# Kernel optimization log

Hardware: AMD Instinct MI355X
Metric: run time of the kernel (lower is better)

Reference implementation:

```python
import jax, jax.numpy as jnp
import numpy as np
from jax import lax

VOCAB = 12000
EMB = 512
RNN = 512
FEATS = 4096
SEQ_LEN = 15


def setup_inputs() -> dict:
    key = jax.random.key(0)
    ks = jax.random.split(key, 10)
    B = 1024
    s = 0.05
    return {
        "img_features": jax.random.normal(ks[0], (B, FEATS), jnp.float32),
        "W_feats": jax.random.normal(ks[1], (EMB, FEATS), jnp.float32) * s,
        "b_feats": jax.random.normal(ks[2], (EMB,), jnp.float32) * s,
        "W_ih": jax.random.normal(ks[3], (4 * RNN, EMB), jnp.float32) * s,
        "W_hh": jax.random.normal(ks[4], (4 * RNN, RNN), jnp.float32) * s,
        "b_ih": jax.random.normal(ks[5], (4 * RNN,), jnp.float32) * s,
        "b_hh": jax.random.normal(ks[6], (4 * RNN,), jnp.float32) * s,
        "emb": jax.random.normal(ks[7], (VOCAB, EMB), jnp.float32) * s,
        "W_out": jax.random.normal(ks[8], (VOCAB - 2, RNN), jnp.float32) * s,
        "b_out": jax.random.normal(ks[9], (VOCAB - 2,), jnp.float32) * s,
    }


def reference(img_features, W_feats, b_feats, W_ih, W_hh, b_ih, b_hh, emb, W_out, b_out):
    B = img_features.shape[0]

    def lstm_cell(x, h, c):
        # torch.nn.LSTMCell: gates ordered i, f, g, o
        gates = x @ W_ih.T + b_ih + h @ W_hh.T + b_hh
        i, f, g, o = jnp.split(gates, 4, axis=1)
        c_new = jax.nn.sigmoid(f) * c + jax.nn.sigmoid(i) * jnp.tanh(g)
        h_new = jax.nn.sigmoid(o) * jnp.tanh(c_new)
        return h_new, c_new

    # image feature embedding + ReLU, then prime the LSTM with it
    img_vec = jax.nn.relu(img_features @ W_feats.T + b_feats)  # [B, 512]
    h = jnp.zeros((B, RNN), img_features.dtype)
    c = jnp.zeros((B, RNN), img_features.dtype)
    h, c = lstm_cell(img_vec, h, c)

    def step(carry, _):
        h, c, words = carry
        x = emb[words]                     # [B, 512] embedding lookup
        h, c = lstm_cell(x, h, c)
        logits = h @ W_out.T + b_out       # [B, VOCAB-2]
        idx = jnp.argmax(logits, axis=1).astype(jnp.int32)
        return (h, c, idx + 2), idx

    words0 = jnp.ones((B,), jnp.int32)  # START token = 1
    _, seq = lax.scan(step, (h, c, words0), None, length=SEQ_LEN)
    return seq.T  # [B, SEQ_LEN] greedy-decoded token ids
```

## Files before the change

### kernel.cpp

```cpp
#include <hip/hip_runtime.h>
#include <stdint.h>

#define BATCH  1024
#define SEQLEN 15
#define NGATE  2048
#define NVOCAB 11998
#define FEATS  4096

typedef __attribute__((ext_vector_type(8)))  short  s8v;
typedef __attribute__((ext_vector_type(16))) float  f32x16;
typedef __attribute__((ext_vector_type(8)))  unsigned short us8;

__device__ __forceinline__ unsigned short f2bf(float f) {
    unsigned u = __float_as_uint(f);
    u += 0x7FFFu + ((u >> 16) & 1u);
    return (unsigned short)(u >> 16);
}
__device__ __forceinline__ float bf2f(unsigned short h) {
    return __uint_as_float(((unsigned)h) << 16);
}
struct bfpair { unsigned short hi, lo; };
__device__ __forceinline__ bfpair split2v(float v) {
    bfpair r;
    r.hi = f2bf(v);
    r.lo = f2bf(v - bf2f(r.hi));
    return r;
}
__device__ __forceinline__ void split8(const float* __restrict__ s, us8& vh, us8& vl) {
    #pragma unroll
    for (int e = 0; e < 8; ++e) {
        bfpair q = split2v(s[e]);
        vh[e] = q.hi; vl[e] = q.lo;
    }
}

__device__ __forceinline__ void async_cp16(const void* g, void* l) {
    __builtin_amdgcn_global_load_lds(
        (const __attribute__((address_space(1))) unsigned int*)g,
        (__attribute__((address_space(3))) unsigned int*)l, 16, 0, 0);
}

__global__ void prep_wcat_blk(const float* __restrict__ W_ih, const float* __restrict__ W_hh,
                              const float* __restrict__ b_ih, const float* __restrict__ b_hh,
                              unsigned short* __restrict__ hi, unsigned short* __restrict__ lo,
                              float* __restrict__ bsum) {
    int idx = blockIdx.x * 256 + threadIdx.x;
    int kc = idx >> 11, row = idx & 2047;
    int k = kc << 3;
    const float* src = (k < 512) ? (W_ih + (size_t)row * 512 + k)
                                 : (W_hh + (size_t)row * 512 + (k - 512));
    us8 vh, vl; split8(src, vh, vl);
    *(us8*)(hi + (size_t)idx * 8) = vh;
    *(us8*)(lo + (size_t)idx * 8) = vl;
    if (idx < NGATE) bsum[idx] = b_ih[idx] + b_hh[idx];
}

__global__ void prep_blk(const float* __restrict__ src,
                         unsigned short* __restrict__ hi, unsigned short* __restrict__ lo,
                         int R, int K) {
    int row = blockIdx.x * 256 + threadIdx.x;
    if (row >= R) return;
    int kc = blockIdx.y;
    us8 vh, vl; split8(src + (size_t)row * K + (kc << 3), vh, vl);
    size_t o = ((size_t)kc * R + row) * 8;
    *(us8*)(hi + o) = vh;
    *(us8*)(lo + o) = vl;
}

__device__ __forceinline__ void mfma_blk_store(
    const unsigned short* __restrict__ Ahi, const unsigned short* __restrict__ Alo, int aRows,
    const unsigned short* __restrict__ Bhi, const unsigned short* __restrict__ Blo, int bRows,
    float* __restrict__ C, int ldc,
    int K, size_t akstride, size_t bkstride, size_t czstride,
    int bm, int bn, int kz)
{
    __shared__ short smem[4 * 4 * 128 * 8];
    short* sAhi = smem;
    short* sAlo = smem + 4 * 128 * 8;
    short* sBhi = smem + 2 * 4 * 128 * 8;
    short* sBlo = smem + 3 * 4 * 128 * 8;

    Ahi += (size_t)kz * akstride;  Alo += (size_t)kz * akstride;
    Bhi += (size_t)kz * bkstride;  Blo += (size_t)kz * bkstride;
    C   += (size_t)kz * czstride;

    const int tid  = threadIdx.x;
    const int lane = tid & 63, wave = tid >> 6;
    const int wr = (wave & 1) * 64, wc = (wave >> 1) * 64;
    const int col = lane & 31, kh = lane >> 5;

    f32x16 acc[2][2] = {};

    for (int k0 = 0; k0 < K; k0 += 32) {
        const int kc0 = k0 >> 3;
        __syncthreads();
        #pragma unroll
        for (int p = 0; p < 2; ++p) {
            int s    = p * 4 + wave;
            int kc_l = s >> 1, rh = s & 1;
            int rl   = rh * 64 + lane;
            int lo_  = (kc_l * 128 + rh * 64) * 8;
            size_t ga = ((size_t)(kc0 + kc_l) * aRows + (bm + rl)) * 8;
            async_cp16(Ahi + ga, sAhi + lo_);
            async_cp16(Alo + ga, sAlo + lo_);
            int brow = bn + rl; if (brow > bRows - 1) brow = bRows - 1;
            size_t gb = ((size_t)(kc0 + kc_l) * bRows + brow) * 8;
            async_cp16(Bhi + gb, sBhi + lo_);
            async_cp16(Blo + gb, sBlo + lo_);
        }
        __syncthreads();

        #pragma unroll
        for (int st = 0; st < 2; ++st) {
            int off = (2 * st + kh) * 128 * 8;
            s8v ah0 = *(const s8v*)(sAhi + off + (wr + col) * 8);
            s8v ah1 = *(const s8v*)(sAhi + off + (wr + 32 + col) * 8);
            s8v al0 = *(const s8v*)(sAlo + off + (wr + col) * 8);
            s8v al1 = *(const s8v*)(sAlo + off + (wr + 32 + col) * 8);
            s8v bh0 = *(const s8v*)(sBhi + off + (wc + col) * 8);
            s8v bh1 = *(const s8v*)(sBhi + off + (wc + 32 + col) * 8);
            s8v bl0 = *(const s8v*)(sBlo + off + (wc + col) * 8);
            s8v bl1 = *(const s8v*)(sBlo + off + (wc + 32 + col) * 8);
            acc[0][0] = __builtin_amdgcn_mfma_f32_32x32x16_bf16(ah0, bh0, acc[0][0], 0, 0, 0);
            acc[0][1] = __builtin_amdgcn_mfma_f32_32x32x16_bf16(ah0, bh1, acc[0][1], 0, 0, 0);
            acc[1][0] = __builtin_amdgcn_mfma_f32_32x32x16_bf16(ah1, bh0, acc[1][0], 0, 0, 0);
            acc[1][1] = __builtin_amdgcn_mfma_f32_32x32x16_bf16(ah1, bh1, acc[1][1], 0, 0, 0);
            acc[0][0] = __builtin_amdgcn_mfma_f32_32x32x16_bf16(ah0, bl0, acc[0][0], 0, 0, 0);
            acc[0][1] = __builtin_amdgcn_mfma_f32_32x32x16_bf16(ah0, bl1, acc[0][1], 0, 0, 0);
            acc[1][0] = __builtin_amdgcn_mfma_f32_32x32x16_bf16(ah1, bl0, acc[1][0], 0, 0, 0);
            acc[1][1] = __builtin_amdgcn_mfma_f32_32x32x16_bf16(ah1, bl1, acc[1][1], 0, 0, 0);
            acc[0][0] = __builtin_amdgcn_mfma_f32_32x32x16_bf16(al0, bh0, acc[0][0], 0, 0, 0);
            acc[0][1] = __builtin_amdgcn_mfma_f32_32x32x16_bf16(al0, bh1, acc[0][1], 0, 0, 0);
            acc[1][0] = __builtin_amdgcn_mfma_f32_32x32x16_bf16(al1, bh0, acc[1][0], 0, 0, 0);
            acc[1][1] = __builtin_amdgcn_mfma_f32_32x32x16_bf16(al1, bh1, acc[1][1], 0, 0, 0);
        }
    }

    #pragma unroll
    for (int i = 0; i < 2; ++i)
        #pragma unroll
        for (int rg = 0; rg < 4; ++rg)
            #pragma unroll
            for (int rr = 0; rr < 4; ++rr) {
                int reg = rg * 4 + rr;
                int m = bm + wr + i * 32 + rr + rg * 8 + kh * 4;
                #pragma unroll
                for (int j = 0; j < 2; ++j) {
                    int n = bn + wc + j * 32 + col;
                    if (n < bRows) C[(size_t)m * ldc + n] = acc[i][j][reg];
                }
            }
}

template<int PPX>
__global__ __launch_bounds__(256) void k_gemm_gates(
    const unsigned short* Ahi, const unsigned short* Alo,
    const unsigned short* Bhi, const unsigned short* Blo,
    float* C, size_t aks, size_t bks, size_t czs) {
    const int l = blockIdx.x, r = l & 7, q = l >> 3;
    const int p = r * PPX + (q >> 3);
    const int mblk = q & 7, nblk = p & 15, kz = p >> 4;
    mfma_blk_store(Ahi, Alo, 1024, Bhi, Blo, NGATE, C, NGATE, 512, aks, bks, czs,
                   mblk * 128, nblk * 128, kz);
}
__global__ __launch_bounds__(256) void k_gemm_feats(
    const unsigned short* Ahi, const unsigned short* Alo,
    const unsigned short* Bhi, const unsigned short* Blo,
    float* C) {
    const int l = blockIdx.x, r = l & 7, q = l >> 3;
    const int p = r * 4 + (q >> 3);
    const int mblk = q & 7, nblk = p & 3, kz = p >> 2;
    mfma_blk_store(Ahi, Alo, 1024, Bhi, Blo, 512, C, 512, 512,
                   (size_t)64 * 1024 * 8, (size_t)64 * 512 * 8, (size_t)1024 * 512,
                   mblk * 128, nblk * 128, kz);
}

__global__ __launch_bounds__(256, 3) void k_logits_argmax(
    const unsigned short* __restrict__ h_hi, const unsigned short* __restrict__ h_lo,
    const unsigned short* __restrict__ wout_hi, const unsigned short* __restrict__ wout_lo,
    const float* __restrict__ bias, unsigned long long* __restrict__ packed)
{
    __shared__ short sB[2][2][4][128][8];

    int mblk, nblk;
    {
        const int l = blockIdx.x, r = l & 7, q = l >> 3;
        if (q < 88) { nblk = r * 11 + (q >> 3); mblk = q & 7; }
        else        { nblk = 88 + (q - 88);     mblk = r;     }
    }

    const int tid  = threadIdx.x;
    const int lane = tid & 63, wave = tid >> 6;
    const int wm = wave & 1, wn = wave >> 1;
    const int col = lane & 31, kh = lane >> 5;
    const int bm = mblk * 128, bn = nblk * 128;
    const int aRows = 1024, bRows = NVOCAB;

    f32x16 acc[2][2] = {};

    auto stage_B = [&](int kcbase, int bufi) {
        #pragma unroll
        for (int p = 0; p < 4; ++p) {
            int s = p * 4 + wave;
            int arr = s >> 3, kc_l = (s >> 1) & 3, rh = s & 1;
            int brow = bn + rh * 64 + lane; if (brow > bRows - 1) brow = bRows - 1;
            size_t gb = ((size_t)(kcbase + kc_l) * bRows + brow) * 8;
            async_cp16((arr ? wout_lo : wout_hi) + gb, &sB[bufi][arr][kc_l][rh * 64][0]);
        }
    };
    auto load_A = [&](int kc0, s8v (&ah)[2][2], s8v (&al)[2][2]) {
        #pragma unroll
        for (int st = 0; st < 2; ++st)
            #pragma unroll
            for (int i = 0; i < 2; ++i) {
                size_t ao = ((size_t)(kc0 + 2 * st + kh) * aRows
                             + (bm + wm * 64 + i * 32 + col)) * 8;
                ah[st][i] = *(const s8v*)(h_hi + ao);
                al[st][i] = *(const s8v*)(h_lo + ao);
            }
    };

    stage_B(0, 0);
    s8v ahc[2][2], alc[2][2], ahn[2][2], aln[2][2];
    load_A(0, ahc, alc);
    __syncthreads();

    int cur = 0;
    for (int ks = 0; ks < 16; ++ks) {
        if (ks + 1 < 16) {
            stage_B((ks + 1) << 2, cur ^ 1);
            load_A((ks + 1) << 2, ahn, aln);
        }

        #pragma unroll
        for (int st = 0; st < 2; ++st) {
            const int kl = 2 * st + kh;
            #pragma unroll
            for (int j = 0; j < 2; ++j) {
                const s8v bh = *(const s8v*)&sB[cur][0][kl][wn * 64 + j * 32 + col][0];
                const s8v bl = *(const s8v*)&sB[cur][1][kl][wn * 64 + j * 32 + col][0];
                #pragma unroll
                for (int i = 0; i < 2; ++i) {
                    acc[i][j] = __builtin_amdgcn_mfma_f32_32x32x16_bf16(ahc[st][i], bh, acc[i][j], 0, 0, 0);
                    acc[i][j] = __builtin_amdgcn_mfma_f32_32x32x16_bf16(ahc[st][i], bl, acc[i][j], 0, 0, 0);
                    acc[i][j] = __builtin_amdgcn_mfma_f32_32x32x16_bf16(alc[st][i], bh, acc[i][j], 0, 0, 0);
                }
            }
        }

        __syncthreads();
        cur ^= 1;
        if (ks + 1 < 16) {
            #pragma unroll
            for (int st = 0; st < 2; ++st)
                #pragma unroll
                for (int i = 0; i < 2; ++i) {
                    ahc[st][i] = ahn[st][i];
                    alc[st][i] = aln[st][i];
                }
        }
    }

    #pragma unroll
    for (int i = 0; i < 2; ++i)
        #pragma unroll
        for (int rg = 0; rg < 4; ++rg)
            #pragma unroll
            for (int rr = 0; rr < 4; ++rr) {
                int reg = rg * 4 + rr;
                int m = bm + wm * 64 + i * 32 + rr + rg * 8 + kh * 4;
                unsigned long long best = 0ull;
                #pragma unroll
                for (int j = 0; j < 2; ++j) {
                    int n = bn + wn * 64 + j * 32 + col;
                    if (n < bRows) {
                        float v = acc[i][j][reg] + bias[n];
                        unsigned int u   = __float_as_uint(v);
                        unsigned int key = (u & 0x80000000u) ? ~u : (u | 0x80000000u);
                        unsigned long long pk =
                            ((unsigned long long)key << 32) |
                            (unsigned long long)(0xFFFFFFFFu - (unsigned)n);
                        best = (pk > best) ? pk : best;
                    }
                }
                #pragma unroll
                for (int sdist = 1; sdist < 32; sdist <<= 1) {
                    unsigned long long o = __shfl_xor(best, sdist, 64);
                    best = (o > best) ? o : best;
                }
                if (col == 0) atomicMax(&packed[m], best);
            }
}

__global__ void feats_reduce8(const float* __restrict__ part, const float* __restrict__ bias,
                              unsigned short* __restrict__ hi, unsigned short* __restrict__ lo) {
    int idx = blockIdx.x * 256 + threadIdx.x;
    int b = idx >> 6, kc = idx & 63;
    int n = kc << 3;
    float v[8];
    #pragma unroll
    for (int e = 0; e < 8; ++e) v[e] = bias[n + e];
    #pragma unroll
    for (int z = 0; z < 8; ++z) {
        const float* s = part + (size_t)z * 1024 * 512 + (size_t)b * 512 + n;
        #pragma unroll
        for (int e = 0; e < 8; ++e) v[e] += s[e];
    }
    us8 vh, vl;
    #pragma unroll
    for (int e = 0; e < 8; ++e) {
        bfpair q = split2v(fmaxf(v[e], 0.f));
        vh[e] = q.hi; vl[e] = q.lo;
    }
    size_t o = ((size_t)kc * 1024 + b) * 8;
    *(us8*)(hi + o) = vh;
    *(us8*)(lo + o) = vl;
}

template<bool PRIME>
__global__ void lstm_pw_blk(const float* __restrict__ g0, const float* __restrict__ g1,
                            const float* __restrict__ bsum, float* __restrict__ cbuf,
                            unsigned short* __restrict__ xh_hi, unsigned short* __restrict__ xh_lo,
                            unsigned long long* __restrict__ packed,
                            int* __restrict__ out, int t) {
    int idx = blockIdx.x * 256 + threadIdx.x;
    int b = idx >> 6, j8 = idx & 63;
    int j = j8 << 3;
    const float* g = g0 + (size_t)b * NGATE;
    float v[4][8];
    #pragma unroll
    for (int gt = 0; gt < 4; ++gt) {
        const float* s = g + gt * 512 + j;
        const float* bs = bsum + gt * 512 + j;
        #pragma unroll
        for (int e = 0; e < 8; ++e) v[gt][e] = s[e] + bs[e];
    }
    if (!PRIME) {
        const float* h2 = g1 + (size_t)b * NGATE;
        #pragma unroll
        for (int gt = 0; gt < 4; ++gt) {
            const float* s = h2 + gt * 512 + j;
            #pragma unroll
            for (int e = 0; e < 8; ++e) v[gt][e] += s[e];
        }
    }
    float* cb = cbuf + (size_t)b * 512 + j;
    us8 vh, vl;
    #pragma unroll
    for (int e = 0; e < 8; ++e) {
        float si = 1.f / (1.f + expf(-v[0][e]));
        float sf = 1.f / (1.f + expf(-v[1][e]));
        float tg = tanhf(v[2][e]);
        float so = 1.f / (1.f + expf(-v[3][e]));
        float cn = PRIME ? (si * tg) : (sf * cb[e] + si * tg);
        cb[e] = cn;
        bfpair q = split2v(so * tanhf(cn));
        vh[e] = q.hi; vl[e] = q.lo;
    }
    size_t o = ((size_t)(64 + j8) * 1024 + b) * 8;
    *(us8*)(xh_hi + o) = vh;
    *(us8*)(xh_lo + o) = vl;
    if (j8 == 0) {
        if (!PRIME && t > 0) {
            unsigned long long p = packed[b];
            out[b * SEQLEN + (t - 1)] = (int)(0xFFFFFFFFu - (unsigned)(p & 0xFFFFFFFFull));
        }
        packed[b] = 0ull;
    }
}

template<int FIRST>
__global__ void gather_blk(const float* __restrict__ emb,
                           const unsigned long long* __restrict__ packed,
                           unsigned short* __restrict__ xh_hi, unsigned short* __restrict__ xh_lo) {
    int idx = blockIdx.x * 256 + threadIdx.x;
    int b = idx >> 6, kc = idx & 63;
    int word = 1;
    if (!FIRST) {
        unsigned long long p = packed[b];
        word = (int)(0xFFFFFFFFu - (unsigned)(p & 0xFFFFFFFFull)) + 2;
    }
    us8 vh, vl; split8(emb + (size_t)word * 512 + (kc << 3), vh, vl);
    size_t o = ((size_t)kc * 1024 + b) * 8;
    *(us8*)(xh_hi + o) = vh;
    *(us8*)(xh_lo + o) = vl;
}

__global__ void final_out(const unsigned long long* __restrict__ packed, int* __restrict__ out) {
    int b = blockIdx.x * 256 + threadIdx.x;
    if (b < BATCH) {
        unsigned long long p = packed[b];
        out[b * SEQLEN + (SEQLEN - 1)] = (int)(0xFFFFFFFFu - (unsigned)(p & 0xFFFFFFFFull));
    }
}

extern "C" void kernel_launch(void* const* d_in, const int* in_sizes, int n_in,
                              void* d_out, int out_size, void* d_ws, size_t ws_size,
                              hipStream_t stream) {
    const float* img     = (const float*)d_in[0];
    const float* W_feats = (const float*)d_in[1];
    const float* b_feats = (const float*)d_in[2];
    const float* W_ih    = (const float*)d_in[3];
    const float* W_hh    = (const float*)d_in[4];
    const float* b_ih    = (const float*)d_in[5];
    const float* b_hh    = (const float*)d_in[6];
    const float* emb     = (const float*)d_in[7];
    const float* W_out   = (const float*)d_in[8];
    const float* b_out   = (const float*)d_in[9];
    int* out = (int*)d_out;

    const size_t WCAT_H = (size_t)128 * 2048 * 8;
    const size_t WOUT_H = (size_t)64 * NVOCAB * 8;
    const size_t XH_H   = (size_t)128 * 1024 * 8;
    const size_t IMGV_H = (size_t)64 * 1024 * 8;

    char* p = (char*)d_ws;
    unsigned short* wcat_hi = (unsigned short*)p;  p += WCAT_H * 2;
    unsigned short* wcat_lo = (unsigned short*)p;  p += WCAT_H * 2;
    unsigned short* wout_hi = (unsigned short*)p;  p += WOUT_H * 2;
    unsigned short* wout_lo = (unsigned short*)p;  p += WOUT_H * 2;
    unsigned short* xh_hi   = (unsigned short*)p;  p += XH_H * 2;
    unsigned short* xh_lo   = (unsigned short*)p;  p += XH_H * 2;
    unsigned short* imgv_hi = (unsigned short*)p;  p += IMGV_H * 2;
    unsigned short* imgv_lo = (unsigned short*)p;  p += IMGV_H * 2;
    float* cbuf             = (float*)p;           p += (size_t)1024 * 512 * 4;
    float* bsum             = (float*)p;           p += (size_t)NGATE * 4;
    unsigned long long* packed = (unsigned long long*)p;  p += (size_t)1024 * 8;
    float* gates0           = (float*)p;           p += (size_t)1024 * NGATE * 4;
    float* gates1           = (float*)p;           p += (size_t)1024 * NGATE * 4;
    unsigned short* imgb_hi = wout_hi;
    unsigned short* imgb_lo = imgb_hi + (size_t)512 * 1024 * 8;
    unsigned short* wfb_hi  = imgb_lo + (size_t)512 * 1024 * 8;
    unsigned short* wfb_lo  = wfb_hi  + (size_t)512 * 512 * 8;
    float* partials = gates0;

    prep_wcat_blk<<<1024, 256, 0, stream>>>(W_ih, W_hh, b_ih, b_hh, wcat_hi, wcat_lo, bsum);
    prep_blk<<<dim3(4, 512), 256, 0, stream>>>(img,     imgb_hi, imgb_lo, 1024, FEATS);
    prep_blk<<<dim3(2, 512), 256, 0, stream>>>(W_feats, wfb_hi,  wfb_lo,  512,  FEATS);

    k_gemm_feats<<<256, 256, 0, stream>>>(imgb_hi, imgb_lo, wfb_hi, wfb_lo, partials);
    feats_reduce8<<<256, 256, 0, stream>>>(partials, b_feats, imgv_hi, imgv_lo);

    prep_blk<<<dim3(47, 64), 256, 0, stream>>>(W_out, wout_hi, wout_lo, NVOCAB, 512);

    k_gemm_gates<2><<<128, 256, 0, stream>>>(imgv_hi, imgv_lo, wcat_hi, wcat_lo,
                                             gates0, 0, 0, 0);
    lstm_pw_blk<true><<<256, 256, 0, stream>>>(gates0, nullptr, bsum, cbuf,
                                               xh_hi, xh_lo, packed, out, 0);

    for (int t = 0; t < SEQLEN; ++t) {
        if (t == 0) gather_blk<1><<<256, 256, 0, stream>>>(emb, packed, xh_hi, xh_lo);
        else        gather_blk<0><<<256, 256, 0, stream>>>(emb, packed, xh_hi, xh_lo);
        k_gemm_gates<4><<<256, 256, 0, stream>>>(
            xh_hi, xh_lo, wcat_hi, wcat_lo, gates0,
            (size_t)64 * 1024 * 8, (size_t)64 * 2048 * 8, (size_t)1024 * NGATE);
        lstm_pw_blk<false><<<256, 256, 0, stream>>>(gates0, gates1, bsum, cbuf,
                                                    xh_hi, xh_lo, packed, out, t);
        k_logits_argmax<<<752, 256, 0, stream>>>(
            xh_hi + (size_t)64 * 1024 * 8, xh_lo + (size_t)64 * 1024 * 8,
            wout_hi, wout_lo, b_out, packed);
    }
    final_out<<<4, 256, 0, stream>>>(packed, out);
}
```

Baseline: 1.620 ms.

## Fuse embedding gather into gates GEMM via pre-split embedding table

Pre-splits the embedding table once into a k-chunked bf16 hi/lo layout, then has the gates GEMM load embedding rows directly through the packed argmax indices for the input half of K. This removes the per-step gather kernel launch and its write/read of the x part of xh. The new path needs extra workspace and falls back to the old path when the workspace is too small. The gathered A rows are scattered, which may hurt load coalescing, and the emb prep kernel adds one-time work.

New measurement: 1.680 ms. 1.04x slower.

```diff
diff --git a/kernel.cpp b/kernel.cpp
--- a/kernel.cpp
+++ b/kernel.cpp
@@ -5,6 +5,7 @@
 #define SEQLEN 15
 #define NGATE  2048
 #define NVOCAB 11998
+#define VOCABSZ 12000
 #define FEATS  4096
 
 typedef __attribute__((ext_vector_type(8)))  short  s8v;
@@ -63,6 +64,16 @@
     int kc = blockIdx.y;
     us8 vh, vl; split8(src + (size_t)row * K + (kc << 3), vh, vl);
     size_t o = ((size_t)kc * R + row) * 8;
+    *(us8*)(hi + o) = vh;
+    *(us8*)(lo + o) = vl;
+}
+
+__global__ void prep_emb_blk(const float* __restrict__ emb,
+                             unsigned short* __restrict__ hi, unsigned short* __restrict__ lo) {
+    int idx = blockIdx.x * 256 + threadIdx.x;
+    int w = idx >> 6, kc = idx & 63;
+    us8 vh, vl; split8(emb + (size_t)w * 512 + (kc << 3), vh, vl);
+    size_t o = ((size_t)kc * VOCABSZ + w) * 8;
     *(us8*)(hi + o) = vh;
     *(us8*)(lo + o) = vl;
 }
@@ -173,6 +184,110 @@
     mfma_blk_store(Ahi, Alo, 1024, Bhi, Blo, 512, C, 512, 512,
                    (size_t)64 * 1024 * 8, (size_t)64 * 512 * 8, (size_t)1024 * 512,
                    mblk * 128, nblk * 128, kz);
+}
+
+__global__ __launch_bounds__(256) void k_gemm_gates_fused(
+    const unsigned short* __restrict__ ebhi, const unsigned short* __restrict__ eblo,
+    const unsigned short* __restrict__ xh_hi, const unsigned short* __restrict__ xh_lo,
+    const unsigned short* __restrict__ wcat_hi, const unsigned short* __restrict__ wcat_lo,
+    const unsigned long long* __restrict__ packed,
+    float* __restrict__ C, int first)
+{
+    __shared__ short smem[4 * 4 * 128 * 8];
+    short* sAhi = smem;
+    short* sAlo = smem + 4 * 128 * 8;
+    short* sBhi = smem + 2 * 4 * 128 * 8;
+    short* sBlo = smem + 3 * 4 * 128 * 8;
+
+    const int l = blockIdx.x, r = l & 7, q = l >> 3;
+    const int p = r * 4 + (q >> 3);
+    const int mblk = q & 7, nblk = p & 15, kz = p >> 4;
+    const int bm = mblk * 128, bn = nblk * 128;
+
+    const int tid  = threadIdx.x;
+    const int lane = tid & 63, wave = tid >> 6;
+    const int wr = (wave & 1) * 64, wc = (wave >> 1) * 64;
+    const int col = lane & 31, kh = lane >> 5;
+    const int rl = (wave & 1) * 64 + lane;
+
+    const unsigned short *Ahi_b, *Alo_b;
+    size_t astr;
+    if (kz == 0) {
+        int wrd = 1;
+        if (!first) {
+            unsigned long long pk = packed[bm + rl];
+            wrd = (int)(0xFFFFFFFFu - (unsigned)(pk & 0xFFFFFFFFull)) + 2;
+        }
+        Ahi_b = ebhi + (size_t)wrd * 8;
+        Alo_b = eblo + (size_t)wrd * 8;
+        astr  = (size_t)VOCABSZ * 8;
+    } else {
+        size_t o = ((size_t)64 * 1024 + bm + rl) * 8;
+        Ahi_b = xh_hi + o;
+        Alo_b = xh_lo + o;
+        astr  = (size_t)1024 * 8;
+    }
+    const unsigned short* Bhi_b = wcat_hi + ((size_t)kz * 64 * NGATE + bn + rl) * 8;
+    const unsigned short* Blo_b = wcat_lo + ((size_t)kz * 64 * NGATE + bn + rl) * 8;
+    C += (size_t)kz * 1024 * NGATE;
+
+    f32x16 acc[2][2] = {};
+
+    for (int k0 = 0; k0 < 512; k0 += 32) {
+        const int kc0 = k0 >> 3;
+        __syncthreads();
+        #pragma unroll
+        for (int pp = 0; pp < 2; ++pp) {
+            int s    = pp * 4 + wave;
+            int kc_l = s >> 1;
+            int lo_  = (kc_l * 128 + (wave & 1) * 64) * 8;
+            async_cp16(Ahi_b + (size_t)(kc0 + kc_l) * astr, sAhi + lo_);
+            async_cp16(Alo_b + (size_t)(kc0 + kc_l) * astr, sAlo + lo_);
+            async_cp16(Bhi_b + (size_t)(kc0 + kc_l) * NGATE * 8, sBhi + lo_);
+            async_cp16(Blo_b + (size_t)(kc0 + kc_l) * NGATE * 8, sBlo + lo_);
+        }
+        __syncthreads();
+
+        #pragma unroll
+        for (int st = 0; st < 2; ++st) {
+            int off = (2 * st + kh) * 128 * 8;
+            s8v ah0 = *(const s8v*)(sAhi + off + (wr + col) * 8);
+            s8v ah1 = *(const s8v*)(sAhi + off + (wr + 32 + col) * 8);
+            s8v al0 = *(const s8v*)(sAlo + off + (wr + col) * 8);
+            s8v al1 = *(const s8v*)(sAlo + off + (wr + 32 + col) * 8);
+            s8v bh0 = *(const s8v*)(sBhi + off + (wc + col) * 8);
+            s8v bh1 = *(const s8v*)(sBhi + off + (wc + 32 + col) * 8);
+            s8v bl0 = *(const s8v*)(sBlo + off + (wc + col) * 8);
+            s8v bl1 = *(const s8v*)(sBlo + off + (wc + 32 + col) * 8);
+            acc[0][0] = __builtin_amdgcn_mfma_f32_32x32x16_bf16(ah0, bh0, acc[0][0], 0, 0, 0);
+            acc[0][1] = __builtin_amdgcn_mfma_f32_32x32x16_bf16(ah0, bh1, acc[0][1], 0, 0, 0);
+            acc[1][0] = __builtin_amdgcn_mfma_f32_32x32x16_bf16(ah1, bh0, acc[1][0], 0, 0, 0);
+            acc[1][1] = __builtin_amdgcn_mfma_f32_32x32x16_bf16(ah1, bh1, acc[1][1], 0, 0, 0);
+            acc[0][0] = __builtin_amdgcn_mfma_f32_32x32x16_bf16(ah0, bl0, acc[0][0], 0, 0, 0);
+            acc[0][1] = __builtin_amdgcn_mfma_f32_32x32x16_bf16(ah0, bl1, acc[0][1], 0, 0, 0);
+            acc[1][0] = __builtin_amdgcn_mfma_f32_32x32x16_bf16(ah1, bl0, acc[1][0], 0, 0, 0);
+            acc[1][1] = __builtin_amdgcn_mfma_f32_32x32x16_bf16(ah1, bl1, acc[1][1], 0, 0, 0);
+            acc[0][0] = __builtin_amdgcn_mfma_f32_32x32x16_bf16(al0, bh0, acc[0][0], 0, 0, 0);
+            acc[0][1] = __builtin_amdgcn_mfma_f32_32x32x16_bf16(al0, bh1, acc[0][1], 0, 0, 0);
+            acc[1][0] = __builtin_amdgcn_mfma_f32_32x32x16_bf16(al1, bh0, acc[1][0], 0, 0, 0);
+            acc[1][1] = __builtin_amdgcn_mfma_f32_32x32x16_bf16(al1, bh1, acc[1][1], 0, 0, 0);
+        }
+    }
+
+    #pragma unroll
+    for (int i = 0; i < 2; ++i)
+        #pragma unroll
+        for (int rg = 0; rg < 4; ++rg)
+            #pragma unroll
+            for (int rr = 0; rr < 4; ++rr) {
+                int reg = rg * 4 + rr;
+                int m = bm + wr + i * 32 + rr + rg * 8 + kh * 4;
+                #pragma unroll
+                for (int j = 0; j < 2; ++j) {
+                    int n = bn + wc + j * 32 + col;
+                    C[(size_t)m * NGATE + n] = acc[i][j][reg];
+                }
+            }
 }
 
 __global__ __launch_bounds__(256, 3) void k_logits_argmax(
@@ -413,6 +528,7 @@
     const size_t WOUT_H = (size_t)64 * NVOCAB * 8;
     const size_t XH_H   = (size_t)128 * 1024 * 8;
     const size_t IMGV_H = (size_t)64 * 1024 * 8;
+    const size_t EMB_H  = (size_t)64 * VOCABSZ * 8;
 
     char* p = (char*)d_ws;
     unsigned short* wcat_hi = (unsigned short*)p;  p += WCAT_H * 2;
@@ -428,6 +544,10 @@
     unsigned long long* packed = (unsigned long long*)p;  p += (size_t)1024 * 8;
     float* gates0           = (float*)p;           p += (size_t)1024 * NGATE * 4;
     float* gates1           = (float*)p;           p += (size_t)1024 * NGATE * 4;
+    unsigned short* ebhi    = (unsigned short*)p;  p += EMB_H * 2;
+    unsigned short* eblo    = (unsigned short*)p;  p += EMB_H * 2;
+    const size_t required = (size_t)(p - (char*)d_ws);
+    const bool fused = (ws_size >= required);
     unsigned short* imgb_hi = wout_hi;
     unsigned short* imgb_lo = imgb_hi + (size_t)512 * 1024 * 8;
     unsigned short* wfb_hi  = imgb_lo + (size_t)512 * 1024 * 8;
@@ -435,6 +555,7 @@
     float* partials = gates0;
 
     prep_wcat_blk<<<1024, 256, 0, stream>>>(W_ih, W_hh, b_ih, b_hh, wcat_hi, wcat_lo, bsum);
+    if (fused) prep_emb_blk<<<3000, 256, 0, stream>>>(emb, ebhi, eblo);
     prep_blk<<<dim3(4, 512), 256, 0, stream>>>(img,     imgb_hi, imgb_lo, 1024, FEATS);
     prep_blk<<<dim3(2, 512), 256, 0, stream>>>(W_feats, wfb_hi,  wfb_lo,  512,  FEATS);
 
@@ -449,11 +570,16 @@
                                                xh_hi, xh_lo, packed, out, 0);
 
     for (int t = 0; t < SEQLEN; ++t) {
-        if (t == 0) gather_blk<1><<<256, 256, 0, stream>>>(emb, packed, xh_hi, xh_lo);
-        else        gather_blk<0><<<256, 256, 0, stream>>>(emb, packed, xh_hi, xh_lo);
-        k_gemm_gates<4><<<256, 256, 0, stream>>>(
-            xh_hi, xh_lo, wcat_hi, wcat_lo, gates0,
-            (size_t)64 * 1024 * 8, (size_t)64 * 2048 * 8, (size_t)1024 * NGATE);
+        if (fused) {
+            k_gemm_gates_fused<<<256, 256, 0, stream>>>(
+                ebhi, eblo, xh_hi, xh_lo, wcat_hi, wcat_lo, packed, gates0, t == 0);
+        } else {
+            if (t == 0) gather_blk<1><<<256, 256, 0, stream>>>(emb, packed, xh_hi, xh_lo);
+            else        gather_blk<0><<<256, 256, 0, stream>>>(emb, packed, xh_hi, xh_lo);
+            k_gemm_gates<4><<<256, 256, 0, stream>>>(
+                xh_hi, xh_lo, wcat_hi, wcat_lo, gates0,
+                (size_t)64 * 1024 * 8, (size_t)64 * 2048 * 8, (size_t)1024 * NGATE);
+        }
         lstm_pw_blk<false><<<256, 256, 0, stream>>>(gates0, gates1, bsum, cbuf,
                                                     xh_hi, xh_lo, packed, out, t);
         k_logits_argmax<<<752, 256, 0, stream>>>(
```
